# Performance work log

Measured on AMD Instinct MI355X. Metric: run time of the kernel, lower is better.

Reference implementation:

```python
import jax, jax.numpy as jnp
import numpy as np

B, S, E, H, D = 2, 2048, 1024, 16, 64

def setup_inputs() -> dict:
    key = jax.random.key(0)
    ks = jax.random.split(key, 6)
    scale = 0.02
    x  = jax.random.normal(ks[0], (B, S, E), dtype=jnp.float32)
    Wq = jax.random.normal(ks[1], (E, E), dtype=jnp.float32) * scale
    Wk = jax.random.normal(ks[2], (E, E), dtype=jnp.float32) * scale
    Wv = jax.random.normal(ks[3], (E, E), dtype=jnp.float32) * scale
    Wo = jax.random.normal(ks[4], (E, E), dtype=jnp.float32) * scale
    bo = jax.random.normal(ks[5], (E,), dtype=jnp.float32) * scale
    return {"x": x, "Wq": Wq, "Wk": Wk, "Wv": Wv, "Wo": Wo, "bo": bo}

def reference(x, Wq, Wk, Wv, Wo, bo):
    # Per-head Q/K/V projections: equivalent to concatenating H heads of size D.
    q = jnp.einsum('bse,ehd->bhsd', x, Wq.reshape(E, H, D))
    k = jnp.einsum('bse,ehd->bhsd', x, Wk.reshape(E, H, D))
    v = jnp.einsum('bse,ehd->bhsd', x, Wv.reshape(E, H, D))
    # Scaled dot-product attention with causal mask (tril), per head.
    scores = jnp.einsum('bhqd,bhkd->bhqk', q, k) * (D ** -0.5)  # [B,H,S,S]
    causal = jnp.tril(jnp.ones((S, S), dtype=bool))
    scores = jnp.where(causal, scores, jnp.float32(-jnp.inf))
    attn = jax.nn.softmax(scores, axis=-1)
    out = jnp.einsum('bhqk,bhkd->bhqd', attn, v)            # [B,H,S,D]
    out = out.transpose(0, 2, 1, 3).reshape(B, S, E)        # concat heads
    # Output projection (dropout prob = 0.0 -> identity).
    return out @ Wo + bo
```

## Files before the change

### kernel.cpp

```cpp
#include <hip/hip_runtime.h>
#include <hip/hip_bf16.h>
#include <cstdint>
#include <cstddef>

typedef unsigned short u16;
typedef unsigned int u32;
typedef __bf16 bf16x8 __attribute__((ext_vector_type(8)));
typedef float f32x4 __attribute__((ext_vector_type(4)));
typedef u32 u32x4 __attribute__((ext_vector_type(4)));
typedef u32 u32x2 __attribute__((ext_vector_type(2)));

constexpr int Bb = 2, Ss = 2048, Ee = 1024, Hh = 16, Dd = 64;
constexpr int Mm = Bb * Ss;
constexpr int NT = Ss / 64;

__device__ __forceinline__ u16 f2bf(float f) {
    union { float f; u32 u; } x; x.f = f;
    u32 r = x.u + 0x7fffu + ((x.u >> 16) & 1u);
    return (u16)(r >> 16);
}

typedef __attribute__((address_space(3))) void lds_void_t;
typedef const __attribute__((address_space(1))) void gbl_void_t;
__device__ __forceinline__ void gload_lds16(const u16* g, u16* l) {
    __builtin_amdgcn_global_load_lds((gbl_void_t*)g, (lds_void_t*)l, 16, 0, 0);
}

__global__ __launch_bounds__(256) void k_pre(
    const float* __restrict__ x,
    const float* __restrict__ Wq, const float* __restrict__ Wk,
    const float* __restrict__ Wv, const float* __restrict__ Wo,
    u16* __restrict__ xb, u16* __restrict__ WqkvT, u16* __restrict__ WoT)
{
    const int z = blockIdx.z;
    const int tx = threadIdx.x, ty = threadIdx.y;
    if (z == 4) {
        const int tid = ty * 32 + tx;
        const size_t base = ((size_t)blockIdx.y * 32 + blockIdx.x) * 4096;
#pragma unroll
        for (int it = 0; it < 4; ++it) {
            const size_t i = base / 4 + it * 256 + tid;
            float4 v = reinterpret_cast<const float4*>(x)[i];
            ushort4 o;
            o.x = f2bf(v.x); o.y = f2bf(v.y); o.z = f2bf(v.z); o.w = f2bf(v.w);
            reinterpret_cast<ushort4*>(xb)[i] = o;
        }
        return;
    }
    __shared__ float sm[32][33];
    const float* src = (z == 0) ? Wq : (z == 1) ? Wk : (z == 2) ? Wv : Wo;
    u16* dst = (z < 3) ? (WqkvT + (size_t)z * Ee * Ee) : WoT;
    const int kt = blockIdx.x * 32, nt = blockIdx.y * 32;
#pragma unroll
    for (int i = 0; i < 4; ++i)
        sm[ty + 8 * i][tx] = src[(size_t)(kt + ty + 8 * i) * Ee + nt + tx];
    __syncthreads();
#pragma unroll
    for (int i = 0; i < 4; ++i)
        dst[(size_t)(nt + ty + 8 * i) * Ee + kt + tx] = f2bf(sm[tx][ty + 8 * i]);
}

template <int MODE>
__global__ __launch_bounds__(256) void k_gemm(
    const u16* __restrict__ A, const u16* __restrict__ Bt,
    void* __restrict__ Cout, u16* __restrict__ vT,
    int K, const float* __restrict__ bias)
{
    __shared__ u16 As[128][32];
    __shared__ u16 Bs[128][32];
    __shared__ u16 Tw[4][16][68];
    const int bm = blockIdx.x * 128, bn = blockIdx.y * 128;
    const int tid = threadIdx.x;
    const int wave = tid >> 6, lane = tid & 63, quad = lane >> 4, l16 = lane & 15;
    const int wr = wave >> 1, wc = wave & 1;

    const int ldrow = lane >> 2, ldcol = (lane & 3) * 8;
    const u16* gA = A + (size_t)(bm + wave * 32 + ldrow) * K + ldcol;
    const u16* gB = Bt + (size_t)(bn + wave * 32 + ldrow) * K + ldcol;
    u16* lA = &As[wave * 32][0];
    u16* lB = &Bs[wave * 32][0];

    f32x4 acc[4][4] = {};

    for (int k0 = 0; k0 < K; k0 += 32) {
        gload_lds16(gA + k0, lA);
        gload_lds16(gA + k0 + 16 * K, lA + 16 * 32);
        gload_lds16(gB + k0, lB);
        gload_lds16(gB + k0 + 16 * K, lB + 16 * 32);
        __syncthreads();

        bf16x8 af[4], bfr[4];
#pragma unroll
        for (int mt = 0; mt < 4; ++mt)
            af[mt] = *reinterpret_cast<bf16x8*>(&As[wr * 64 + mt * 16 + l16][quad * 8]);
#pragma unroll
        for (int nt = 0; nt < 4; ++nt)
            bfr[nt] = *reinterpret_cast<bf16x8*>(&Bs[wc * 64 + nt * 16 + l16][quad * 8]);
#pragma unroll
        for (int mt = 0; mt < 4; ++mt)
#pragma unroll
            for (int nt = 0; nt < 4; ++nt)
                acc[mt][nt] = __builtin_amdgcn_mfma_f32_16x16x32_bf16(
                    af[mt], bfr[nt], acc[mt][nt], 0, 0, 0);
        __syncthreads();
    }

    if constexpr (MODE == 1) {
        float* C = (float*)Cout;
#pragma unroll
        for (int mt = 0; mt < 4; ++mt)
#pragma unroll
            for (int nt = 0; nt < 4; ++nt) {
                const int col = bn + wc * 64 + nt * 16 + l16;
                const float bv = bias[col];
#pragma unroll
                for (int r = 0; r < 4; ++r) {
                    const int row = bm + wr * 64 + mt * 16 + quad * 4 + r;
                    C[(size_t)row * Ee + col] = acc[mt][nt][r] + bv;
                }
            }
    } else {
        if (bn < 2 * Ee) {
            u16* C = (u16*)Cout;
#pragma unroll
            for (int mt = 0; mt < 4; ++mt)
#pragma unroll
                for (int nt = 0; nt < 4; ++nt) {
                    const int col = bn + wc * 64 + nt * 16 + l16;
#pragma unroll
                    for (int r = 0; r < 4; ++r) {
                        const int row = bm + wr * 64 + mt * 16 + quad * 4 + r;
                        C[(size_t)row * (2 * Ee) + col] = f2bf(acc[mt][nt][r]);
                    }
                }
        } else {
            const int m_base = bm + wr * 64;
            const int b = m_base >> 11, s0 = m_base & 2047;
            const int rw = lane >> 2, cg = (lane & 3) * 16;
#pragma unroll
            for (int nt = 0; nt < 4; ++nt) {
#pragma unroll
                for (int mt = 0; mt < 4; ++mt)
#pragma unroll
                    for (int r = 0; r < 4; ++r)
                        Tw[wave][l16][mt * 16 + quad * 4 + r] = f2bf(acc[mt][nt][r]);
                __asm__ volatile("s_waitcnt lgkmcnt(0)" ::: "memory");
                const int vd = bn - 2 * Ee + wc * 64 + nt * 16 + rw;
                u16* dst = vT + ((size_t)(b * Hh + (vd >> 6)) * Dd + (vd & 63)) * Ss + s0 + cg;
                int4 a0 = *reinterpret_cast<int4*>(&Tw[wave][rw][cg]);
                int4 a1 = *reinterpret_cast<int4*>(&Tw[wave][rw][cg + 8]);
                *reinterpret_cast<int4*>(dst) = a0;
                *reinterpret_cast<int4*>(dst + 8) = a1;
                __asm__ volatile("s_waitcnt lgkmcnt(0)" ::: "memory");
            }
        }
    }
}

__global__ __launch_bounds__(256) void k_attn(
    const u16* __restrict__ qk, const u16* __restrict__ vT,
    u16* __restrict__ attn_out)
{
    __shared__ u16 Qs[64][72];
    __shared__ u16 Ks[2][64][72];
    __shared__ u16 Vs[2][64][72];

    const int pair = blockIdx.x;
    const int bh = blockIdx.y;
    const int b = bh >> 4, h = bh & 15;
    const int tid = threadIdx.x;
    const int wave = tid >> 6, lane = tid & 63, quad = lane >> 4, l16 = lane & 15;
    const int r8 = tid >> 3, g8 = tid & 7;
    const size_t qkbase = (size_t)b * Ss * (2 * Ee);
    const size_t vbase  = ((size_t)(b * Hh + h) * Dd) * Ss;

    const int tiles[2] = { pair, NT - 1 - pair };
    constexpr float LOG2E = 1.4426950408889634f;
    constexpr float C1 = 0.125f * LOG2E;
    constexpr float C2 = 4.0f * LOG2E;

    for (int ph = 0; ph < 2; ++ph) {
        const int qt = tiles[ph];

#pragma unroll
        for (int hf = 0; hf < 2; ++hf) {
            const int rr = r8 + hf * 32;
            *reinterpret_cast<int4*>(&Qs[rr][g8 * 8]) = *reinterpret_cast<const int4*>(
                qk + qkbase + (size_t)(qt * 64 + rr) * (2 * Ee) + h * 64 + g8 * 8);
            *reinterpret_cast<int4*>(&Ks[0][rr][g8 * 8]) = *reinterpret_cast<const int4*>(
                qk + qkbase + (size_t)rr * (2 * Ee) + Ee + h * 64 + g8 * 8);
            *reinterpret_cast<int4*>(&Vs[0][rr][g8 * 8]) = *reinterpret_cast<const int4*>(
                vT + vbase + (size_t)rr * Ss + g8 * 8);
        }
        __syncthreads();

        const bf16x8 aq0 = *reinterpret_cast<bf16x8*>(&Qs[wave * 16 + l16][quad * 8]);
        const bf16x8 aq1 = *reinterpret_cast<bf16x8*>(&Qs[wave * 16 + l16][32 + quad * 8]);

        float l_lane = 0.f;
        f32x4 acc[4];
#pragma unroll
        for (int dt = 0; dt < 4; ++dt) acc[dt] = (f32x4){0.f, 0.f, 0.f, 0.f};

        for (int kt = 0; kt <= qt; ++kt) {
            const int cur = kt & 1, nxt = cur ^ 1;
            int4 kreg0, kreg1, vreg0, vreg1;
            if (kt < qt) {
                kreg0 = *reinterpret_cast<const int4*>(
                    qk + qkbase + (size_t)((kt + 1) * 64 + r8) * (2 * Ee) + Ee + h * 64 + g8 * 8);
                kreg1 = *reinterpret_cast<const int4*>(
                    qk + qkbase + (size_t)((kt + 1) * 64 + r8 + 32) * (2 * Ee) + Ee + h * 64 + g8 * 8);
                vreg0 = *reinterpret_cast<const int4*>(
                    vT + vbase + (size_t)r8 * Ss + (kt + 1) * 64 + g8 * 8);
                vreg1 = *reinterpret_cast<const int4*>(
                    vT + vbase + (size_t)(r8 + 32) * Ss + (kt + 1) * 64 + g8 * 8);
            }

            f32x4 sc[4];
#pragma unroll
            for (int ct = 0; ct < 4; ++ct) {
                bf16x8 bk0 = *reinterpret_cast<bf16x8*>(&Ks[cur][ct * 16 + l16][quad * 8]);
                bf16x8 bk1 = *reinterpret_cast<bf16x8*>(&Ks[cur][ct * 16 + l16][32 + quad * 8]);
                f32x4 z = {0.f, 0.f, 0.f, 0.f};
                z = __builtin_amdgcn_mfma_f32_16x16x32_bf16(bk0, aq0, z, 0, 0, 0);
                z = __builtin_amdgcn_mfma_f32_16x16x32_bf16(bk1, aq1, z, 0, 0, 0);
                sc[ct] = z;
            }

            u32 pb[4][4];
            if (kt == qt) {
#pragma unroll
                for (int ct = 0; ct < 4; ++ct)
#pragma unroll
                    for (int r = 0; r < 4; ++r) {
                        float t = sc[ct][r] * C1 - C2;
                        if (ct * 16 + quad * 4 + r > wave * 16 + l16) t = -INFINITY;
                        union { float f; u32 u; } p; p.f = exp2f(t);
                        pb[ct][r] = p.u & 0xffff0000u;
                        p.u = pb[ct][r];
                        l_lane += p.f;
                    }
            } else {
#pragma unroll
                for (int ct = 0; ct < 4; ++ct)
#pragma unroll
                    for (int r = 0; r < 4; ++r) {
                        union { float f; u32 u; } p; p.f = exp2f(sc[ct][r] * C1 - C2);
                        pb[ct][r] = p.u & 0xffff0000u;
                        p.u = pb[ct][r];
                        l_lane += p.f;
                    }
            }

#pragma unroll
            for (int p2 = 0; p2 < 2; ++p2) {
                u32x4 bw;
                bw[0] = (pb[2 * p2][0] >> 16) | pb[2 * p2][1];
                bw[1] = (pb[2 * p2][2] >> 16) | pb[2 * p2][3];
                bw[2] = (pb[2 * p2 + 1][0] >> 16) | pb[2 * p2 + 1][1];
                bw[3] = (pb[2 * p2 + 1][2] >> 16) | pb[2 * p2 + 1][3];
                const bf16x8 pf = __builtin_bit_cast(bf16x8, bw);
#pragma unroll
                for (int dt = 0; dt < 4; ++dt) {
                    u32x2 lo = *reinterpret_cast<u32x2*>(&Vs[cur][dt * 16 + l16][p2 * 32 + quad * 4]);
                    u32x2 hi = *reinterpret_cast<u32x2*>(&Vs[cur][dt * 16 + l16][p2 * 32 + 16 + quad * 4]);
                    u32x4 aw = {lo[0], lo[1], hi[0], hi[1]};
                    const bf16x8 vf = __builtin_bit_cast(bf16x8, aw);
                    acc[dt] = __builtin_amdgcn_mfma_f32_16x16x32_bf16(vf, pf, acc[dt], 0, 0, 0);
                }
            }

            if (kt < qt) {
                *reinterpret_cast<int4*>(&Ks[nxt][r8][g8 * 8]) = kreg0;
                *reinterpret_cast<int4*>(&Ks[nxt][r8 + 32][g8 * 8]) = kreg1;
                *reinterpret_cast<int4*>(&Vs[nxt][r8][g8 * 8]) = vreg0;
                *reinterpret_cast<int4*>(&Vs[nxt][r8 + 32][g8 * 8]) = vreg1;
            }
            __syncthreads();
        }

        l_lane += __shfl_xor(l_lane, 16);
        l_lane += __shfl_xor(l_lane, 32);
        const float inv = 1.0f / l_lane;
        const int row = qt * 64 + wave * 16 + l16;
#pragma unroll
        for (int dt = 0; dt < 4; ++dt) {
            ushort4 o;
            o.x = f2bf(acc[dt][0] * inv);
            o.y = f2bf(acc[dt][1] * inv);
            o.z = f2bf(acc[dt][2] * inv);
            o.w = f2bf(acc[dt][3] * inv);
            *reinterpret_cast<ushort4*>(
                &attn_out[((size_t)b * Ss + row) * Ee + h * 64 + dt * 16 + quad * 4]) = o;
        }
    }
}

extern "C" void kernel_launch(void* const* d_in, const int* in_sizes, int n_in,
                              void* d_out, int out_size, void* d_ws, size_t ws_size,
                              hipStream_t stream)
{
    const float* x  = (const float*)d_in[0];
    const float* Wq = (const float*)d_in[1];
    const float* Wk = (const float*)d_in[2];
    const float* Wv = (const float*)d_in[3];
    const float* Wo = (const float*)d_in[4];
    const float* bo = (const float*)d_in[5];
    float* out = (float*)d_out;

    u16* xb    = (u16*)d_ws;
    u16* WqkvT = xb + (size_t)Mm * Ee;
    u16* WoT   = WqkvT + (size_t)3 * Ee * Ee;
    u16* qk    = WoT + (size_t)Ee * Ee;
    u16* vT    = qk + (size_t)Mm * 2 * Ee;
    u16* attn  = vT + (size_t)Bb * Hh * Dd * Ss;
    const size_t need = ((size_t)Mm * Ee + (size_t)3 * Ee * Ee + (size_t)Ee * Ee +
                         (size_t)Mm * 2 * Ee + (size_t)Bb * Hh * Dd * Ss +
                         (size_t)Mm * Ee) * sizeof(u16);
    if (ws_size < need) return;

    k_pre<<<dim3(32, 32, 5), dim3(32, 8), 0, stream>>>(x, Wq, Wk, Wv, Wo, xb, WqkvT, WoT);
    k_gemm<2><<<dim3(Mm / 128, 3 * Ee / 128), 256, 0, stream>>>(xb, WqkvT, qk, vT, Ee, nullptr);
    k_attn<<<dim3(NT / 2, Bb * Hh), 256, 0, stream>>>(qk, vT, attn);
    k_gemm<1><<<dim3(Mm / 128, Ee / 128), 256, 0, stream>>>(attn, WoT, out, nullptr, Ee, bo);
}
```

Before: 190.0 us.

## Restructure attention to adjacent query-tile pairs sharing K/V, split output GEMM tiles

The attention kernel now runs 512-thread blocks in which two groups of four waves handle adjacent query tiles and share each streamed K/V tile. Blocks are reordered so long and short tiles are interleaved, and Q fragments are read straight from global memory rather than staged in LDS. V is written to LDS in a permuted layout so each fragment comes from a single 16-byte read. The output projection gets its own kernel with 128x64 tiles, which doubles the block count for better occupancy. This aims to cut redundant K/V traffic and balance load, at the cost of idle waves in the first group on the last tile and more register pressure.

```diff
diff --git a/kernel.cpp b/kernel.cpp
--- a/kernel.cpp
+++ b/kernel.cpp
@@ -60,11 +60,9 @@
         dst[(size_t)(nt + ty + 8 * i) * Ee + kt + tx] = f2bf(sm[tx][ty + 8 * i]);
 }
 
-template <int MODE>
-__global__ __launch_bounds__(256) void k_gemm(
+__global__ __launch_bounds__(256) void k_gemmqkv(
     const u16* __restrict__ A, const u16* __restrict__ Bt,
-    void* __restrict__ Cout, u16* __restrict__ vT,
-    int K, const float* __restrict__ bias)
+    u16* __restrict__ qkout, u16* __restrict__ vT)
 {
     __shared__ u16 As[128][32];
     __shared__ u16 Bs[128][32];
@@ -75,18 +73,18 @@
     const int wr = wave >> 1, wc = wave & 1;
 
     const int ldrow = lane >> 2, ldcol = (lane & 3) * 8;
-    const u16* gA = A + (size_t)(bm + wave * 32 + ldrow) * K + ldcol;
-    const u16* gB = Bt + (size_t)(bn + wave * 32 + ldrow) * K + ldcol;
+    const u16* gA = A + (size_t)(bm + wave * 32 + ldrow) * Ee + ldcol;
+    const u16* gB = Bt + (size_t)(bn + wave * 32 + ldrow) * Ee + ldcol;
     u16* lA = &As[wave * 32][0];
     u16* lB = &Bs[wave * 32][0];
 
     f32x4 acc[4][4] = {};
 
-    for (int k0 = 0; k0 < K; k0 += 32) {
+    for (int k0 = 0; k0 < Ee; k0 += 32) {
         gload_lds16(gA + k0, lA);
-        gload_lds16(gA + k0 + 16 * K, lA + 16 * 32);
+        gload_lds16(gA + k0 + 16 * Ee, lA + 16 * 32);
         gload_lds16(gB + k0, lB);
-        gload_lds16(gB + k0 + 16 * K, lB + 16 * 32);
+        gload_lds16(gB + k0 + 16 * Ee, lB + 16 * 32);
         __syncthreads();
 
         bf16x8 af[4], bfr[4];
@@ -105,117 +103,152 @@
         __syncthreads();
     }
 
-    if constexpr (MODE == 1) {
-        float* C = (float*)Cout;
+    if (bn < 2 * Ee) {
 #pragma unroll
         for (int mt = 0; mt < 4; ++mt)
 #pragma unroll
             for (int nt = 0; nt < 4; ++nt) {
                 const int col = bn + wc * 64 + nt * 16 + l16;
-                const float bv = bias[col];
 #pragma unroll
                 for (int r = 0; r < 4; ++r) {
                     const int row = bm + wr * 64 + mt * 16 + quad * 4 + r;
-                    C[(size_t)row * Ee + col] = acc[mt][nt][r] + bv;
+                    qkout[(size_t)row * (2 * Ee) + col] = f2bf(acc[mt][nt][r]);
                 }
             }
     } else {
-        if (bn < 2 * Ee) {
-            u16* C = (u16*)Cout;
+        const int m_base = bm + wr * 64;
+        const int b = m_base >> 11, s0 = m_base & 2047;
+        const int rw = lane >> 2, cg = (lane & 3) * 16;
+#pragma unroll
+        for (int nt = 0; nt < 4; ++nt) {
 #pragma unroll
             for (int mt = 0; mt < 4; ++mt)
 #pragma unroll
-                for (int nt = 0; nt < 4; ++nt) {
-                    const int col = bn + wc * 64 + nt * 16 + l16;
-#pragma unroll
-                    for (int r = 0; r < 4; ++r) {
-                        const int row = bm + wr * 64 + mt * 16 + quad * 4 + r;
-                        C[(size_t)row * (2 * Ee) + col] = f2bf(acc[mt][nt][r]);
-                    }
-                }
-        } else {
-            const int m_base = bm + wr * 64;
-            const int b = m_base >> 11, s0 = m_base & 2047;
-            const int rw = lane >> 2, cg = (lane & 3) * 16;
-#pragma unroll
-            for (int nt = 0; nt < 4; ++nt) {
-#pragma unroll
-                for (int mt = 0; mt < 4; ++mt)
-#pragma unroll
-                    for (int r = 0; r < 4; ++r)
-                        Tw[wave][l16][mt * 16 + quad * 4 + r] = f2bf(acc[mt][nt][r]);
-                __asm__ volatile("s_waitcnt lgkmcnt(0)" ::: "memory");
-                const int vd = bn - 2 * Ee + wc * 64 + nt * 16 + rw;
-                u16* dst = vT + ((size_t)(b * Hh + (vd >> 6)) * Dd + (vd & 63)) * Ss + s0 + cg;
-                int4 a0 = *reinterpret_cast<int4*>(&Tw[wave][rw][cg]);
-                int4 a1 = *reinterpret_cast<int4*>(&Tw[wave][rw][cg + 8]);
-                *reinterpret_cast<int4*>(dst) = a0;
-                *reinterpret_cast<int4*>(dst + 8) = a1;
-                __asm__ volatile("s_waitcnt lgkmcnt(0)" ::: "memory");
-            }
-        }
-    }
-}
-
-__global__ __launch_bounds__(256) void k_attn(
+                for (int r = 0; r < 4; ++r)
+                    Tw[wave][l16][mt * 16 + quad * 4 + r] = f2bf(acc[mt][nt][r]);
+            __asm__ volatile("s_waitcnt lgkmcnt(0)" ::: "memory");
+            const int vd = bn - 2 * Ee + wc * 64 + nt * 16 + rw;
+            u16* dst = vT + ((size_t)(b * Hh + (vd >> 6)) * Dd + (vd & 63)) * Ss + s0 + cg;
+            int4 a0 = *reinterpret_cast<int4*>(&Tw[wave][rw][cg]);
+            int4 a1 = *reinterpret_cast<int4*>(&Tw[wave][rw][cg + 8]);
+            *reinterpret_cast<int4*>(dst) = a0;
+            *reinterpret_cast<int4*>(dst + 8) = a1;
+            __asm__ volatile("s_waitcnt lgkmcnt(0)" ::: "memory");
+        }
+    }
+}
+
+__global__ __launch_bounds__(256) void k_gemmo(
+    const u16* __restrict__ A, const u16* __restrict__ Bt,
+    float* __restrict__ C, const float* __restrict__ bias)
+{
+    __shared__ u16 As[128][32];
+    __shared__ u16 Bs[64][32];
+    const int bm = blockIdx.x * 128, bn = blockIdx.y * 64;
+    const int tid = threadIdx.x;
+    const int wave = tid >> 6, lane = tid & 63, quad = lane >> 4, l16 = lane & 15;
+    const int ldrow = lane >> 2, ldcol = (lane & 3) * 8;
+    const u16* gA = A + (size_t)(bm + wave * 32 + ldrow) * Ee + ldcol;
+    const u16* gB = Bt + (size_t)(bn + wave * 16 + ldrow) * Ee + ldcol;
+    u16* lA = &As[wave * 32][0];
+    u16* lB = &Bs[wave * 16][0];
+
+    f32x4 acc[2][4] = {};
+
+    for (int k0 = 0; k0 < Ee; k0 += 32) {
+        gload_lds16(gA + k0, lA);
+        gload_lds16(gA + k0 + 16 * Ee, lA + 16 * 32);
+        gload_lds16(gB + k0, lB);
+        __syncthreads();
+
+        bf16x8 af[2], bfr[4];
+#pragma unroll
+        for (int mt = 0; mt < 2; ++mt)
+            af[mt] = *reinterpret_cast<bf16x8*>(&As[wave * 32 + mt * 16 + l16][quad * 8]);
+#pragma unroll
+        for (int nt = 0; nt < 4; ++nt)
+            bfr[nt] = *reinterpret_cast<bf16x8*>(&Bs[nt * 16 + l16][quad * 8]);
+#pragma unroll
+        for (int mt = 0; mt < 2; ++mt)
+#pragma unroll
+            for (int nt = 0; nt < 4; ++nt)
+                acc[mt][nt] = __builtin_amdgcn_mfma_f32_16x16x32_bf16(
+                    af[mt], bfr[nt], acc[mt][nt], 0, 0, 0);
+        __syncthreads();
+    }
+
+#pragma unroll
+    for (int mt = 0; mt < 2; ++mt)
+#pragma unroll
+        for (int nt = 0; nt < 4; ++nt) {
+            const int col = bn + nt * 16 + l16;
+            const float bv = bias[col];
+#pragma unroll
+            for (int r = 0; r < 4; ++r) {
+                const int row = bm + wave * 32 + mt * 16 + quad * 4 + r;
+                C[(size_t)row * Ee + col] = acc[mt][nt][r] + bv;
+            }
+        }
+}
+
+__global__ __launch_bounds__(512) void k_attn(
     const u16* __restrict__ qk, const u16* __restrict__ vT,
     u16* __restrict__ attn_out)
 {
-    __shared__ u16 Qs[64][72];
     __shared__ u16 Ks[2][64][72];
     __shared__ u16 Vs[2][64][72];
 
-    const int pair = blockIdx.x;
-    const int bh = blockIdx.y;
+    const int beta = blockIdx.x;
+    const int bh = beta & 31;
+    const int m = beta >> 5;
+    const int i = (m >> 3) ? 15 - (m & 7) : (m & 7);
+    const int qtA = 2 * i, qtB = 2 * i + 1;
     const int b = bh >> 4, h = bh & 15;
     const int tid = threadIdx.x;
     const int wave = tid >> 6, lane = tid & 63, quad = lane >> 4, l16 = lane & 15;
+    const int grp = wave >> 2, w4 = wave & 3;
+    const int qt = grp ? qtB : qtA;
     const int r8 = tid >> 3, g8 = tid & 7;
+    const int vb = (g8 >> 2) * 32 + (g8 & 1) * 16 + ((g8 >> 1) & 1) * 4;
     const size_t qkbase = (size_t)b * Ss * (2 * Ee);
     const size_t vbase  = ((size_t)(b * Hh + h) * Dd) * Ss;
 
-    const int tiles[2] = { pair, NT - 1 - pair };
     constexpr float LOG2E = 1.4426950408889634f;
     constexpr float C1 = 0.125f * LOG2E;
     constexpr float C2 = 4.0f * LOG2E;
 
-    for (int ph = 0; ph < 2; ++ph) {
-        const int qt = tiles[ph];
-
-#pragma unroll
-        for (int hf = 0; hf < 2; ++hf) {
-            const int rr = r8 + hf * 32;
-            *reinterpret_cast<int4*>(&Qs[rr][g8 * 8]) = *reinterpret_cast<const int4*>(
-                qk + qkbase + (size_t)(qt * 64 + rr) * (2 * Ee) + h * 64 + g8 * 8);
-            *reinterpret_cast<int4*>(&Ks[0][rr][g8 * 8]) = *reinterpret_cast<const int4*>(
-                qk + qkbase + (size_t)rr * (2 * Ee) + Ee + h * 64 + g8 * 8);
-            *reinterpret_cast<int4*>(&Vs[0][rr][g8 * 8]) = *reinterpret_cast<const int4*>(
-                vT + vbase + (size_t)rr * Ss + g8 * 8);
-        }
-        __syncthreads();
-
-        const bf16x8 aq0 = *reinterpret_cast<bf16x8*>(&Qs[wave * 16 + l16][quad * 8]);
-        const bf16x8 aq1 = *reinterpret_cast<bf16x8*>(&Qs[wave * 16 + l16][32 + quad * 8]);
-
-        float l_lane = 0.f;
-        f32x4 acc[4];
-#pragma unroll
-        for (int dt = 0; dt < 4; ++dt) acc[dt] = (f32x4){0.f, 0.f, 0.f, 0.f};
-
-        for (int kt = 0; kt <= qt; ++kt) {
-            const int cur = kt & 1, nxt = cur ^ 1;
-            int4 kreg0, kreg1, vreg0, vreg1;
-            if (kt < qt) {
-                kreg0 = *reinterpret_cast<const int4*>(
-                    qk + qkbase + (size_t)((kt + 1) * 64 + r8) * (2 * Ee) + Ee + h * 64 + g8 * 8);
-                kreg1 = *reinterpret_cast<const int4*>(
-                    qk + qkbase + (size_t)((kt + 1) * 64 + r8 + 32) * (2 * Ee) + Ee + h * 64 + g8 * 8);
-                vreg0 = *reinterpret_cast<const int4*>(
-                    vT + vbase + (size_t)r8 * Ss + (kt + 1) * 64 + g8 * 8);
-                vreg1 = *reinterpret_cast<const int4*>(
-                    vT + vbase + (size_t)(r8 + 32) * Ss + (kt + 1) * 64 + g8 * 8);
-            }
-
+    const u16* qrow = qk + qkbase + (size_t)(qt * 64 + w4 * 16 + l16) * (2 * Ee) + h * 64;
+    const bf16x8 aq0 = *reinterpret_cast<const bf16x8*>(qrow + quad * 8);
+    const bf16x8 aq1 = *reinterpret_cast<const bf16x8*>(qrow + 32 + quad * 8);
+
+    {
+        int4 k0 = *reinterpret_cast<const int4*>(
+            qk + qkbase + (size_t)r8 * (2 * Ee) + Ee + h * 64 + g8 * 8);
+        int4 v0 = *reinterpret_cast<const int4*>(
+            vT + vbase + (size_t)r8 * Ss + g8 * 8);
+        *reinterpret_cast<int4*>(&Ks[0][r8][g8 * 8]) = k0;
+        u32x2 lo = {(u32)v0.x, (u32)v0.y}, hi = {(u32)v0.z, (u32)v0.w};
+        *reinterpret_cast<u32x2*>(&Vs[0][r8][vb]) = lo;
+        *reinterpret_cast<u32x2*>(&Vs[0][r8][vb + 8]) = hi;
+    }
+    __syncthreads();
+
+    float l_lane = 0.f;
+    f32x4 acc[4];
+#pragma unroll
+    for (int dt = 0; dt < 4; ++dt) acc[dt] = (f32x4){0.f, 0.f, 0.f, 0.f};
+
+    for (int kt = 0; kt <= qtB; ++kt) {
+        const int cur = kt & 1, nxt = cur ^ 1;
+        int4 kreg, vreg;
+        if (kt < qtB) {
+            kreg = *reinterpret_cast<const int4*>(
+                qk + qkbase + (size_t)((kt + 1) * 64 + r8) * (2 * Ee) + Ee + h * 64 + g8 * 8);
+            vreg = *reinterpret_cast<const int4*>(
+                vT + vbase + (size_t)r8 * Ss + (kt + 1) * 64 + g8 * 8);
+        }
+
+        if (kt <= qt) {
             f32x4 sc[4];
 #pragma unroll
             for (int ct = 0; ct < 4; ++ct) {
@@ -234,7 +267,7 @@
 #pragma unroll
                     for (int r = 0; r < 4; ++r) {
                         float t = sc[ct][r] * C1 - C2;
-                        if (ct * 16 + quad * 4 + r > wave * 16 + l16) t = -INFINITY;
+                        if (ct * 16 + quad * 4 + r > w4 * 16 + l16) t = -INFINITY;
                         union { float f; u32 u; } p; p.f = exp2f(t);
                         pb[ct][r] = p.u & 0xffff0000u;
                         p.u = pb[ct][r];
@@ -262,37 +295,35 @@
                 const bf16x8 pf = __builtin_bit_cast(bf16x8, bw);
 #pragma unroll
                 for (int dt = 0; dt < 4; ++dt) {
-                    u32x2 lo = *reinterpret_cast<u32x2*>(&Vs[cur][dt * 16 + l16][p2 * 32 + quad * 4]);
-                    u32x2 hi = *reinterpret_cast<u32x2*>(&Vs[cur][dt * 16 + l16][p2 * 32 + 16 + quad * 4]);
-                    u32x4 aw = {lo[0], lo[1], hi[0], hi[1]};
-                    const bf16x8 vf = __builtin_bit_cast(bf16x8, aw);
+                    const bf16x8 vf = *reinterpret_cast<bf16x8*>(
+                        &Vs[cur][dt * 16 + l16][p2 * 32 + quad * 8]);
                     acc[dt] = __builtin_amdgcn_mfma_f32_16x16x32_bf16(vf, pf, acc[dt], 0, 0, 0);
                 }
             }
-
-            if (kt < qt) {
-                *reinterpret_cast<int4*>(&Ks[nxt][r8][g8 * 8]) = kreg0;
-                *reinterpret_cast<int4*>(&Ks[nxt][r8 + 32][g8 * 8]) = kreg1;
-                *reinterpret_cast<int4*>(&Vs[nxt][r8][g8 * 8]) = vreg0;
-                *reinterpret_cast<int4*>(&Vs[nxt][r8 + 32][g8 * 8]) = vreg1;
-            }
-            __syncthreads();
-        }
-
-        l_lane += __shfl_xor(l_lane, 16);
-        l_lane += __shfl_xor(l_lane, 32);
-        const float inv = 1.0f / l_lane;
-        const int row = qt * 64 + wave * 16 + l16;
-#pragma unroll
-        for (int dt = 0; dt < 4; ++dt) {
-            ushort4 o;
-            o.x = f2bf(acc[dt][0] * inv);
-            o.y = f2bf(acc[dt][1] * inv);
-            o.z = f2bf(acc[dt][2] * inv);
-            o.w = f2bf(acc[dt][3] * inv);
-            *reinterpret_cast<ushort4*>(
-                &attn_out[((size_t)b * Ss + row) * Ee + h * 64 + dt * 16 + quad * 4]) = o;
-        }
+        }
+
+        if (kt < qtB) {
+            *reinterpret_cast<int4*>(&Ks[nxt][r8][g8 * 8]) = kreg;
+            u32x2 lo = {(u32)vreg.x, (u32)vreg.y}, hi = {(u32)vreg.z, (u32)vreg.w};
+            *reinterpret_cast<u32x2*>(&Vs[nxt][r8][vb]) = lo;
+            *reinterpret_cast<u32x2*>(&Vs[nxt][r8][vb + 8]) = hi;
+        }
+        __syncthreads();
+    }
+
+    l_lane += __shfl_xor(l_lane, 16);
+    l_lane += __shfl_xor(l_lane, 32);
+    const float inv = 1.0f / l_lane;
+    const int row = qt * 64 + w4 * 16 + l16;
+#pragma unroll
+    for (int dt = 0; dt < 4; ++dt) {
+        ushort4 o;
+        o.x = f2bf(acc[dt][0] * inv);
+        o.y = f2bf(acc[dt][1] * inv);
+        o.z = f2bf(acc[dt][2] * inv);
+        o.w = f2bf(acc[dt][3] * inv);
+        *reinterpret_cast<ushort4*>(
+            &attn_out[((size_t)b * Ss + row) * Ee + h * 64 + dt * 16 + quad * 4]) = o;
     }
 }
 
@@ -320,7 +351,7 @@
     if (ws_size < need) return;
 
     k_pre<<<dim3(32, 32, 5), dim3(32, 8), 0, stream>>>(x, Wq, Wk, Wv, Wo, xb, WqkvT, WoT);
-    k_gemm<2><<<dim3(Mm / 128, 3 * Ee / 128), 256, 0, stream>>>(xb, WqkvT, qk, vT, Ee, nullptr);
-    k_attn<<<dim3(NT / 2, Bb * Hh), 256, 0, stream>>>(qk, vT, attn);
-    k_gemm<1><<<dim3(Mm / 128, Ee / 128), 256, 0, stream>>>(attn, WoT, out, nullptr, Ee, bo);
-}
+    k_gemmqkv<<<dim3(Mm / 128, 3 * Ee / 128), 256, 0, stream>>>(xb, WqkvT, qk, vT);
+    k_attn<<<dim3(512), 512, 0, stream>>>(qk, vT, attn);
+    k_gemmo<<<dim3(Mm / 128, Ee / 64), 256, 0, stream>>>(attn, WoT, out, bo);
+}
```

Result: no change. 191.0 us (+0.5%).
